# Optimization experiments

Hardware: AMD Instinct MI355X
Metric: run time of the kernel (lower is better)

Reference implementation:

```python
import jax, jax.numpy as jnp
import numpy as np

N_HEADS = 8
D_HEAD = 16
D_IN = 128
N_NODES = 50000
N_EDGES = 600000


def setup_inputs() -> dict:
    key = jax.random.key(0)
    ks = jax.random.split(key, 7)
    x = jax.random.normal(ks[0], (N_NODES, D_IN), dtype=jnp.float32)
    edge_attr = jax.random.normal(ks[1], (N_EDGES, D_IN), dtype=jnp.float32)
    edge_index = jax.random.randint(ks[2], (2, N_EDGES), 0, N_NODES, dtype=jnp.int32)
    # Linear weights stored as [in, out] so projection is x @ W.
    s = 1.0 / np.sqrt(D_IN)
    WQ = jax.random.normal(ks[3], (D_IN, N_HEADS * D_HEAD), dtype=jnp.float32) * s
    WK = jax.random.normal(ks[4], (D_IN, N_HEADS * D_HEAD), dtype=jnp.float32) * s
    WV = jax.random.normal(ks[5], (D_IN, N_HEADS * D_HEAD), dtype=jnp.float32) * s
    WE = jax.random.normal(ks[6], (D_IN, N_HEADS * D_HEAD), dtype=jnp.float32) * s
    return {"x": x, "edge_attr": edge_attr, "edge_index": edge_index,
            "WQ": WQ, "WK": WK, "WV": WV, "WE": WE}


def reference(x, edge_attr, edge_index, WQ, WK, WV, WE):
    N = x.shape[0]
    q = (x @ WQ).reshape(N, N_HEADS, D_HEAD)
    k = (x @ WK).reshape(N, N_HEADS, D_HEAD)
    v = (x @ WV).reshape(N, N_HEADS, D_HEAD)
    e_proj = (edge_attr @ WE).reshape(-1, N_HEADS, D_HEAD)
    row, col = edge_index[0], edge_index[1]
    # per-edge gather-compute: [E, H, D]
    alpha = (k[row] * q[col]) * (1.0 / np.sqrt(D_HEAD))
    alpha = jnp.clip(alpha, -5.0, 5.0) * e_proj
    e_out = alpha  # update_edge_feats=True
    alphax = jnp.exp(jnp.clip(alpha.sum(-1, keepdims=True), -5.0, 5.0))  # [E, H, 1]
    wV = jax.ops.segment_sum(v[row] * alphax, col, num_segments=N)  # [N, H, D]
    z = jax.ops.segment_sum(alphax, col, num_segments=N)            # [N, H, 1]
    h_out = wV / (z + 1e-6)
    return h_out, e_out
```

## Files before the change

### kernel.cpp

```cpp
#include <hip/hip_runtime.h>

#define DIN 128
#define NHEADS 8
#define DHEAD 16
#define NPB 32
#define EPB 64

typedef __attribute__((ext_vector_type(8))) short short8;
typedef __attribute__((ext_vector_type(4))) float f32x4;

__device__ __forceinline__ float clip5(float x) {
    return fminf(fmaxf(x, -5.0f), 5.0f);
}

__device__ __forceinline__ unsigned short f2bf(float f) {
    unsigned u = __float_as_uint(f);
    unsigned r = (u + 0x7FFF + ((u >> 16) & 1)) >> 16;
    return (unsigned short)r;
}

__device__ __forceinline__ float b2f(unsigned short u) {
    return __uint_as_float((unsigned)u << 16);
}

__device__ __forceinline__ float bflo(unsigned u) {
    return __uint_as_float(u << 16);
}
__device__ __forceinline__ float bfhi(unsigned u) {
    return __uint_as_float(u & 0xffff0000u);
}


__device__ __forceinline__ void tile_gemm(const float xs[][DIN], int r0, int cg,
                                          const float* __restrict__ W,
                                          float4 acc[4]) {
#pragma unroll 4
    for (int kk = 0; kk < DIN; kk += 4) {
        float4 a[4];
#pragma unroll
        for (int i = 0; i < 4; ++i)
            a[i] = *(const float4*)&xs[r0 + i][kk];
#pragma unroll
        for (int t = 0; t < 4; ++t) {
            float4 w = *(const float4*)&W[(kk + t) * DIN + (cg << 2)];
#pragma unroll
            for (int i = 0; i < 4; ++i) {
                float av = ((const float*)&a[i])[t];
                acc[i].x = fmaf(av, w.x, acc[i].x);
                acc[i].y = fmaf(av, w.y, acc[i].y);
                acc[i].z = fmaf(av, w.z, acc[i].z);
                acc[i].w = fmaf(av, w.w, acc[i].w);
            }
        }
    }
}

__global__ __launch_bounds__(256) void node_proj_kernel(
    const float* __restrict__ x, const float* __restrict__ WQ,
    const float* __restrict__ WK, const float* __restrict__ WV,
    unsigned short* __restrict__ qbf, unsigned short* __restrict__ kbf,
    unsigned short* __restrict__ vbf, int N) {
    __shared__ float xs[NPB][DIN];
    const int tid = threadIdx.x;
    const int n0 = blockIdx.x * NPB;

#pragma unroll
    for (int i = 0; i < NPB * DIN / (256 * 4); ++i) {
        int idx = (tid + i * 256) * 4;
        int r = idx / DIN, c = idx % DIN;
        float4 val = make_float4(0.f, 0.f, 0.f, 0.f);
        if (n0 + r < N) val = *(const float4*)&x[(long)(n0 + r) * DIN + c];
        *(float4*)&xs[r][c] = val;
    }
    __syncthreads();

    const int cg = tid & 31;
    const int ng = tid >> 5;
    const int r0 = ng * 4;

    const float* Ws[3] = {WQ, WK, WV};
    unsigned short* outs[3] = {qbf, kbf, vbf};
#pragma unroll
    for (int m = 0; m < 3; ++m) {
        float4 acc[4] = {make_float4(0,0,0,0), make_float4(0,0,0,0),
                         make_float4(0,0,0,0), make_float4(0,0,0,0)};
        tile_gemm(xs, r0, cg, Ws[m], acc);
#pragma unroll
        for (int i = 0; i < 4; ++i) {
            int n = n0 + r0 + i;
            if (n < N) {
                ushort4 b;
                b.x = f2bf(acc[i].x); b.y = f2bf(acc[i].y);
                b.z = f2bf(acc[i].z); b.w = f2bf(acc[i].w);
                *(ushort4*)&outs[m][(long)n * DIN + (cg << 2)] = b;
            }
        }
    }
}


__global__ __launch_bounds__(256) void degree_kernel(
    const int* __restrict__ cols, int* __restrict__ deg, int E) {
    int e = blockIdx.x * 256 + threadIdx.x;
    if (e < E) atomicAdd(&deg[cols[e]], 1);
}

__global__ __launch_bounds__(256) void block_sum_kernel(
    const int* __restrict__ deg, int* __restrict__ bsum, int N) {
    __shared__ int s[256];
    int tid = threadIdx.x;
    int i = blockIdx.x * 256 + tid;
    s[tid] = (i < N) ? deg[i] : 0;
    __syncthreads();
    for (int st = 128; st > 0; st >>= 1) {
        if (tid < st) s[tid] += s[tid + st];
        __syncthreads();
    }
    if (tid == 0) bsum[blockIdx.x] = s[0];
}

__global__ __launch_bounds__(256) void scan_bsum_kernel(int* __restrict__ bsum, int NB) {
    __shared__ int s[256];
    int tid = threadIdx.x;
    int v = (tid < NB) ? bsum[tid] : 0;
    s[tid] = v;
    __syncthreads();
    for (int off = 1; off < 256; off <<= 1) {
        int t = (tid >= off) ? s[tid - off] : 0;
        __syncthreads();
        s[tid] += t;
        __syncthreads();
    }
    if (tid < NB) bsum[tid] = s[tid] - v;
}

__global__ __launch_bounds__(256) void offsets_kernel(
    const int* __restrict__ deg, const int* __restrict__ bsumscan,
    int* __restrict__ offsets, int* __restrict__ cursor, int N, int E) {
    __shared__ int s[256];
    int tid = threadIdx.x;
    int i = blockIdx.x * 256 + tid;
    int v = (i < N) ? deg[i] : 0;
    s[tid] = v;
    __syncthreads();
    for (int off = 1; off < 256; off <<= 1) {
        int t = (tid >= off) ? s[tid - off] : 0;
        __syncthreads();
        s[tid] += t;
        __syncthreads();
    }
    int excl = s[tid] - v + bsumscan[blockIdx.x];
    if (i < N) { offsets[i] = excl; cursor[i] = excl; }
    if (blockIdx.x == 0 && tid == 0) offsets[N] = E;
}

__global__ __launch_bounds__(256) void scatter_kernel(
    const int* __restrict__ rows, const int* __restrict__ cols,
    int* __restrict__ cursor, int* __restrict__ elist,
    int* __restrict__ rows_s, int* __restrict__ cols_s, int E) {
    int e = blockIdx.x * 256 + threadIdx.x;
    if (e >= E) return;
    int c = cols[e];
    int pos = atomicAdd(&cursor[c], 1);
    elist[pos] = e;
    rows_s[pos] = rows[e];
    cols_s[pos] = c;
}


__global__ __launch_bounds__(256) void prep_wet_kernel(
    const float* __restrict__ WE, unsigned short* __restrict__ WEt) {
    int idx = blockIdx.x * 256 + threadIdx.x;
    int kk = idx >> 7, n = idx & 127;
    WEt[n * DIN + kk] = f2bf(WE[kk * DIN + n]);
}


__global__ __launch_bounds__(256) void edge_mfma_kernel(
    const float* __restrict__ edge_attr, const int* __restrict__ elist,
    const int* __restrict__ rows_s, const int* __restrict__ cols_s,
    const unsigned short* __restrict__ WEt, const unsigned short* __restrict__ qbf,
    const unsigned short* __restrict__ kbf, float* __restrict__ e_out,
    float* __restrict__ ax_s, int E) {
    const int tid = threadIdx.x;
    const int e0 = blockIdx.x * EPB;
    const int w = tid >> 6;
    const int l = tid & 63;
    const int lr = l & 15;
    const int lg = l >> 4;
    const int j = e0 + w * 16 + lr;
    const long eg = elist[j];
    const int er = rows_s[j];
    const int ec = cols_s[j];

    const float* arow = &edge_attr[eg * DIN + lg * 8];
    f32x4 ea[8];
#pragma unroll
    for (int ks = 0; ks < 4; ++ks) {
        ea[ks * 2]     = __builtin_nontemporal_load((const f32x4*)&arow[ks * 32]);
        ea[ks * 2 + 1] = __builtin_nontemporal_load((const f32x4*)&arow[ks * 32 + 4]);
    }
    const unsigned short* krow = &kbf[(long)er * DIN + lg * 4];
    const unsigned short* qrow = &qbf[(long)ec * DIN + lg * 4];
    ushort4 kv[8], qv[8];
#pragma unroll
    for (int ft = 0; ft < 8; ++ft) {
        kv[ft] = *(const ushort4*)&krow[ft * 16];
        qv[ft] = *(const ushort4*)&qrow[ft * 16];
    }
    __builtin_amdgcn_sched_barrier(0);

    short8 bfrag[4];
#pragma unroll
    for (int ks = 0; ks < 4; ++ks) {
        f32x4 a0 = ea[ks * 2], a1 = ea[ks * 2 + 1];
        short8 f;
        f[0] = (short)f2bf(a0[0]); f[1] = (short)f2bf(a0[1]);
        f[2] = (short)f2bf(a0[2]); f[3] = (short)f2bf(a0[3]);
        f[4] = (short)f2bf(a1[0]); f[5] = (short)f2bf(a1[1]);
        f[6] = (short)f2bf(a1[2]); f[7] = (short)f2bf(a1[3]);
        bfrag[ks] = f;
    }

#pragma unroll
    for (int ft = 0; ft < 8; ++ft) {
        f32x4 acc = (f32x4){0.f, 0.f, 0.f, 0.f};
#pragma unroll
        for (int ks = 0; ks < 4; ++ks) {
            short8 af = *(const short8*)&WEt[(ft * 16 + lr) * DIN + ks * 32 + lg * 8];
            acc = __builtin_amdgcn_mfma_f32_16x16x32_bf16(af, bfrag[ks], acc, 0, 0, 0);
        }
        const int f0 = ft * 16 + lg * 4;
        f32x4 t;
        t[0] = clip5(b2f(kv[ft].x) * b2f(qv[ft].x) * 0.25f) * acc[0];
        t[1] = clip5(b2f(kv[ft].y) * b2f(qv[ft].y) * 0.25f) * acc[1];
        t[2] = clip5(b2f(kv[ft].z) * b2f(qv[ft].z) * 0.25f) * acc[2];
        t[3] = clip5(b2f(kv[ft].w) * b2f(qv[ft].w) * 0.25f) * acc[3];
        __builtin_nontemporal_store(t, (f32x4*)&e_out[eg * DIN + f0]);

        float s = t[0] + t[1] + t[2] + t[3];
        s += __shfl_xor(s, 16);
        s += __shfl_xor(s, 32);
        float axv = __expf(clip5(s));
        if (lg == 0)
            ax_s[(long)j * NHEADS + ft] = axv;
    }
}


__global__ __launch_bounds__(256) void aggregate_kernel(
    const int* __restrict__ offsets, const int* __restrict__ rows_s,
    const float* __restrict__ ax_s, const unsigned short* __restrict__ vbf,
    float* __restrict__ h_out, int N) {
    int wid = blockIdx.x * 4 + (threadIdx.x >> 6);
    int lane = threadIdx.x & 63;
    if (wid >= N) return;
    int beg = offsets[wid], end = offsets[wid + 1];
    const int head = lane >> 3;

    float2 acc = make_float2(0.f, 0.f);
    float zacc = 0.f;

    for (int j = beg; j < end; j += 8) {
        int n = end - j; n = (n > 8) ? 8 : n;
        int r_[8]; float a_[8]; unsigned u_[8];
#pragma unroll
        for (int t = 0; t < 8; ++t)
            r_[t] = rows_s[j + ((t < n) ? t : 0)];
#pragma unroll
        for (int t = 0; t < 8; ++t) {
            a_[t] = (t < n) ? ax_s[(long)(j + t) * NHEADS + head] : 0.f;
            u_[t] = *(const unsigned*)&vbf[(long)r_[t] * DIN + lane * 2];
        }
#pragma unroll
        for (int t = 0; t < 8; ++t) {
            acc.x = fmaf(bflo(u_[t]), a_[t], acc.x);
            acc.y = fmaf(bfhi(u_[t]), a_[t], acc.y);
            zacc += a_[t];
        }
    }
    float inv = 1.0f / (zacc + 1e-6f);
    float2 res = make_float2(acc.x * inv, acc.y * inv);
    *(float2*)&h_out[(long)wid * DIN + lane * 2] = res;
}

extern "C" void kernel_launch(void* const* d_in, const int* in_sizes, int n_in,
                              void* d_out, int out_size, void* d_ws, size_t ws_size,
                              hipStream_t stream) {
    const float* x         = (const float*)d_in[0];
    const float* edge_attr = (const float*)d_in[1];
    const int*   edge_index= (const int*)d_in[2];
    const float* WQ        = (const float*)d_in[3];
    const float* WK        = (const float*)d_in[4];
    const float* WV        = (const float*)d_in[5];
    const float* WE        = (const float*)d_in[6];

    const int N = in_sizes[0] / DIN;
    const int E = in_sizes[2] / 2;
    const int NB = (N + 255) / 256;

    float* out   = (float*)d_out;
    float* h_out = out;
    float* e_out = out + (long)N * DIN;

    unsigned short* qbf = (unsigned short*)d_ws;
    unsigned short* kbf = qbf + (long)N * DIN;
    unsigned short* vbf = kbf + (long)N * DIN;
    float* ax_s = (float*)(vbf + (long)N * DIN);
    unsigned short* WEt = (unsigned short*)(ax_s + (long)E * NHEADS);
    int* ip      = (int*)(WEt + DIN * DIN);
    int* deg     = ip;
    int* cursor  = deg + N;
    int* offsets = cursor + N;
    int* bsum    = offsets + N + 1;
    int* elist   = bsum + 256;
    int* rows_s  = elist + E;
    int* cols_s  = rows_s + E;

    const int* rows = edge_index;
    const int* cols = edge_index + E;

    hipMemsetAsync(deg, 0, (size_t)N * sizeof(int), stream);

    node_proj_kernel<<<(N + NPB - 1) / NPB, 256, 0, stream>>>(x, WQ, WK, WV, qbf, kbf, vbf, N);
    prep_wet_kernel<<<DIN * DIN / 256, 256, 0, stream>>>(WE, WEt);

    degree_kernel<<<(E + 255) / 256, 256, 0, stream>>>(cols, deg, E);
    block_sum_kernel<<<NB, 256, 0, stream>>>(deg, bsum, N);
    scan_bsum_kernel<<<1, 256, 0, stream>>>(bsum, NB);
    offsets_kernel<<<NB, 256, 0, stream>>>(deg, bsum, offsets, cursor, N, E);
    scatter_kernel<<<(E + 255) / 256, 256, 0, stream>>>(rows, cols, cursor,
                                                        elist, rows_s, cols_s, E);

    edge_mfma_kernel<<<E / EPB, 256, 0, stream>>>(
        edge_attr, elist, rows_s, cols_s, WEt, qbf, kbf, e_out, ax_s, E);

    aggregate_kernel<<<(N + 3) / 4, 256, 0, stream>>>(
        offsets, rows_s, ax_s, vbf, h_out, N);
}
```

Measured before the change: 485.7 us.

## Software-pipeline edge MFMA kernel over four 16-edge chunks per wave

Each wave now handles 64 edges in four chunks of 16, double-buffering registers so the gathers of edge_attr, K and Q for the next chunk are issued while the current chunk runs its MFMA and epilogue. Index loads are prefetched two chunks ahead, and the block size per launch grows from 64 to 256 edges, with launch bounds asking for two blocks per SIMD. The aim is to hide gather latency inside each wave instead of relying on occupancy. The cost is higher register pressure from the double buffers, which could cause spills or lower occupancy, plus fewer blocks in the grid.

```diff
diff --git a/kernel.cpp b/kernel.cpp
--- a/kernel.cpp
+++ b/kernel.cpp
@@ -4,7 +4,7 @@
 #define NHEADS 8
 #define DHEAD 16
 #define NPB 32
-#define EPB 64
+#define EPB 256
 
 typedef __attribute__((ext_vector_type(8))) short short8;
 typedef __attribute__((ext_vector_type(4))) float f32x4;
@@ -176,7 +176,7 @@
 }
 
 
-__global__ __launch_bounds__(256) void edge_mfma_kernel(
+__global__ __launch_bounds__(256, 2) void edge_mfma_kernel(
     const float* __restrict__ edge_attr, const int* __restrict__ elist,
     const int* __restrict__ rows_s, const int* __restrict__ cols_s,
     const unsigned short* __restrict__ WEt, const unsigned short* __restrict__ qbf,
@@ -188,63 +188,96 @@
     const int l = tid & 63;
     const int lr = l & 15;
     const int lg = l >> 4;
-    const int j = e0 + w * 16 + lr;
-    const long eg = elist[j];
-    const int er = rows_s[j];
-    const int ec = cols_s[j];
-
-    const float* arow = &edge_attr[eg * DIN + lg * 8];
-    f32x4 ea[8];
-#pragma unroll
-    for (int ks = 0; ks < 4; ++ks) {
-        ea[ks * 2]     = __builtin_nontemporal_load((const f32x4*)&arow[ks * 32]);
-        ea[ks * 2 + 1] = __builtin_nontemporal_load((const f32x4*)&arow[ks * 32 + 4]);
-    }
-    const unsigned short* krow = &kbf[(long)er * DIN + lg * 4];
-    const unsigned short* qrow = &qbf[(long)ec * DIN + lg * 4];
-    ushort4 kv[8], qv[8];
-#pragma unroll
-    for (int ft = 0; ft < 8; ++ft) {
-        kv[ft] = *(const ushort4*)&krow[ft * 16];
-        qv[ft] = *(const ushort4*)&qrow[ft * 16];
-    }
+    const int jbase = e0 + w * 64;
+
+    bool valid[4];
+    int eg_[4], er_[4], ec_[4];
+    f32x4 ea_[2][8];
+    ushort4 kv_[2][8], qv_[2][8];
+
+#pragma unroll
+    for (int c = 0; c < 4; ++c) valid[c] = (jbase + c * 16) < E;
+
+#define IDX_LOAD(c)                                                  \
+    if (valid[c]) {                                                  \
+        int j = jbase + (c) * 16 + lr;                               \
+        eg_[c] = elist[j]; er_[c] = rows_s[j]; ec_[c] = cols_s[j];   \
+    }
+
+#define DATA_LOAD(s, c)                                              \
+    if (valid[c]) {                                                  \
+        const float* arow = &edge_attr[(long)eg_[c] * DIN + lg * 8]; \
+        _Pragma("unroll")                                            \
+        for (int ks = 0; ks < 4; ++ks) {                             \
+            ea_[s][ks * 2]     = __builtin_nontemporal_load((const f32x4*)&arow[ks * 32]);     \
+            ea_[s][ks * 2 + 1] = __builtin_nontemporal_load((const f32x4*)&arow[ks * 32 + 4]); \
+        }                                                            \
+        const unsigned short* krow = &kbf[(long)er_[c] * DIN + lg * 4]; \
+        const unsigned short* qrow = &qbf[(long)ec_[c] * DIN + lg * 4]; \
+        _Pragma("unroll")                                            \
+        for (int ft = 0; ft < 8; ++ft) {                             \
+            kv_[s][ft] = *(const ushort4*)&krow[ft * 16];            \
+            qv_[s][ft] = *(const ushort4*)&qrow[ft * 16];            \
+        }                                                            \
+    }
+
+    IDX_LOAD(0)
+    IDX_LOAD(1)
     __builtin_amdgcn_sched_barrier(0);
-
-    short8 bfrag[4];
-#pragma unroll
-    for (int ks = 0; ks < 4; ++ks) {
-        f32x4 a0 = ea[ks * 2], a1 = ea[ks * 2 + 1];
-        short8 f;
-        f[0] = (short)f2bf(a0[0]); f[1] = (short)f2bf(a0[1]);
-        f[2] = (short)f2bf(a0[2]); f[3] = (short)f2bf(a0[3]);
-        f[4] = (short)f2bf(a1[0]); f[5] = (short)f2bf(a1[1]);
-        f[6] = (short)f2bf(a1[2]); f[7] = (short)f2bf(a1[3]);
-        bfrag[ks] = f;
-    }
-
-#pragma unroll
-    for (int ft = 0; ft < 8; ++ft) {
-        f32x4 acc = (f32x4){0.f, 0.f, 0.f, 0.f};
-#pragma unroll
-        for (int ks = 0; ks < 4; ++ks) {
-            short8 af = *(const short8*)&WEt[(ft * 16 + lr) * DIN + ks * 32 + lg * 8];
-            acc = __builtin_amdgcn_mfma_f32_16x16x32_bf16(af, bfrag[ks], acc, 0, 0, 0);
-        }
-        const int f0 = ft * 16 + lg * 4;
-        f32x4 t;
-        t[0] = clip5(b2f(kv[ft].x) * b2f(qv[ft].x) * 0.25f) * acc[0];
-        t[1] = clip5(b2f(kv[ft].y) * b2f(qv[ft].y) * 0.25f) * acc[1];
-        t[2] = clip5(b2f(kv[ft].z) * b2f(qv[ft].z) * 0.25f) * acc[2];
-        t[3] = clip5(b2f(kv[ft].w) * b2f(qv[ft].w) * 0.25f) * acc[3];
-        __builtin_nontemporal_store(t, (f32x4*)&e_out[eg * DIN + f0]);
-
-        float s = t[0] + t[1] + t[2] + t[3];
-        s += __shfl_xor(s, 16);
-        s += __shfl_xor(s, 32);
-        float axv = __expf(clip5(s));
-        if (lg == 0)
-            ax_s[(long)j * NHEADS + ft] = axv;
-    }
+    DATA_LOAD(0, 0)
+    __builtin_amdgcn_sched_barrier(0);
+
+#pragma unroll
+    for (int c = 0; c < 4; ++c) {
+        const int s = c & 1;
+        if (c + 2 < 4) { IDX_LOAD(c + 2) }
+        if (c + 1 < 4) { DATA_LOAD((c + 1) & 1, c + 1) }
+        __builtin_amdgcn_sched_barrier(0);
+
+        if (valid[c]) {
+            const int j = jbase + c * 16 + lr;
+            const long eg = eg_[c];
+
+            short8 bfrag[4];
+#pragma unroll
+            for (int ks = 0; ks < 4; ++ks) {
+                f32x4 a0 = ea_[s][ks * 2], a1 = ea_[s][ks * 2 + 1];
+                short8 f;
+                f[0] = (short)f2bf(a0[0]); f[1] = (short)f2bf(a0[1]);
+                f[2] = (short)f2bf(a0[2]); f[3] = (short)f2bf(a0[3]);
+                f[4] = (short)f2bf(a1[0]); f[5] = (short)f2bf(a1[1]);
+                f[6] = (short)f2bf(a1[2]); f[7] = (short)f2bf(a1[3]);
+                bfrag[ks] = f;
+            }
+
+#pragma unroll
+            for (int ft = 0; ft < 8; ++ft) {
+                f32x4 acc = (f32x4){0.f, 0.f, 0.f, 0.f};
+#pragma unroll
+                for (int ks = 0; ks < 4; ++ks) {
+                    short8 af = *(const short8*)&WEt[(ft * 16 + lr) * DIN + ks * 32 + lg * 8];
+                    acc = __builtin_amdgcn_mfma_f32_16x16x32_bf16(af, bfrag[ks], acc, 0, 0, 0);
+                }
+                const int f0 = ft * 16 + lg * 4;
+                f32x4 t;
+                t[0] = clip5(b2f(kv_[s][ft].x) * b2f(qv_[s][ft].x) * 0.25f) * acc[0];
+                t[1] = clip5(b2f(kv_[s][ft].y) * b2f(qv_[s][ft].y) * 0.25f) * acc[1];
+                t[2] = clip5(b2f(kv_[s][ft].z) * b2f(qv_[s][ft].z) * 0.25f) * acc[2];
+                t[3] = clip5(b2f(kv_[s][ft].w) * b2f(qv_[s][ft].w) * 0.25f) * acc[3];
+                __builtin_nontemporal_store(t, (f32x4*)&e_out[eg * DIN + f0]);
+
+                float sum = t[0] + t[1] + t[2] + t[3];
+                sum += __shfl_xor(sum, 16);
+                sum += __shfl_xor(sum, 32);
+                float axv = __expf(clip5(sum));
+                if (lg == 0)
+                    ax_s[(long)j * NHEADS + ft] = axv;
+            }
+        }
+        __builtin_amdgcn_sched_barrier(0);
+    }
+#undef IDX_LOAD
+#undef DATA_LOAD
 }
 
 
@@ -332,7 +365,7 @@
     scatter_kernel<<<(E + 255) / 256, 256, 0, stream>>>(rows, cols, cursor,
                                                         elist, rows_s, cols_s, E);
 
-    edge_mfma_kernel<<<E / EPB, 256, 0, stream>>>(
+    edge_mfma_kernel<<<(E + EPB - 1) / EPB, 256, 0, stream>>>(
         edge_attr, elist, rows_s, cols_s, WEt, qbf, kbf, e_out, ax_s, E);
 
     aggregate_kernel<<<(N + 3) / 4, 256, 0, stream>>>(
```

Result: slower. 500.6 us (+3.1%).

## Split aggregate wave into four edge sub-groups with 16-byte V loads

Applied to the files above, without the earlier changes.

The aggregation kernel now has each wave split into four 16-lane sub-groups. Each sub-group handles different edges of the node and loads a full 16-byte chunk of the bf16 V row per lane, instead of all 64 lanes reading 4 bytes from the same edge. Partial sums are combined with cross-lane shuffles, and one sub-group writes the output, which adds an early path for nodes with no edges. The aim is fewer, wider gather loads and fewer serial loop iterations per node, at the cost of a shuffle reduction and idle lanes during the store.

```diff
diff --git a/kernel.cpp b/kernel.cpp
--- a/kernel.cpp
+++ b/kernel.cpp
@@ -256,32 +256,60 @@
     int lane = threadIdx.x & 63;
     if (wid >= N) return;
     int beg = offsets[wid], end = offsets[wid + 1];
-    const int head = lane >> 3;
-
-    float2 acc = make_float2(0.f, 0.f);
+    const int sub = lane >> 4;
+    const int f16 = lane & 15;
+    const int head = f16 >> 1;
+
+    if (beg == end) {
+        if (sub == 0) {
+            f32x4 zz = (f32x4){0.f, 0.f, 0.f, 0.f};
+            *(f32x4*)&h_out[(long)wid * DIN + f16 * 8] = zz;
+            *(f32x4*)&h_out[(long)wid * DIN + f16 * 8 + 4] = zz;
+        }
+        return;
+    }
+
+    float acc[8] = {0.f, 0.f, 0.f, 0.f, 0.f, 0.f, 0.f, 0.f};
     float zacc = 0.f;
 
     for (int j = beg; j < end; j += 8) {
-        int n = end - j; n = (n > 8) ? 8 : n;
-        int r_[8]; float a_[8]; unsigned u_[8];
-#pragma unroll
-        for (int t = 0; t < 8; ++t)
-            r_[t] = rows_s[j + ((t < n) ? t : 0)];
-#pragma unroll
-        for (int t = 0; t < 8; ++t) {
-            a_[t] = (t < n) ? ax_s[(long)(j + t) * NHEADS + head] : 0.f;
-            u_[t] = *(const unsigned*)&vbf[(long)r_[t] * DIN + lane * 2];
-        }
-#pragma unroll
-        for (int t = 0; t < 8; ++t) {
-            acc.x = fmaf(bflo(u_[t]), a_[t], acc.x);
-            acc.y = fmaf(bfhi(u_[t]), a_[t], acc.y);
-            zacc += a_[t];
-        }
-    }
-    float inv = 1.0f / (zacc + 1e-6f);
-    float2 res = make_float2(acc.x * inv, acc.y * inv);
-    *(float2*)&h_out[(long)wid * DIN + lane * 2] = res;
+        int n = end - j;
+        bool v0 = sub < n, v1 = 4 + sub < n;
+        int jj0 = v0 ? (j + sub) : beg;
+        int jj1 = v1 ? (j + 4 + sub) : beg;
+        int r0 = rows_s[jj0], r1 = rows_s[jj1];
+        float a0 = v0 ? ax_s[(long)jj0 * NHEADS + head] : 0.f;
+        float a1 = v1 ? ax_s[(long)jj1 * NHEADS + head] : 0.f;
+        uint4 u0 = *(const uint4*)&vbf[(long)r0 * DIN + f16 * 8];
+        uint4 u1 = *(const uint4*)&vbf[(long)r1 * DIN + f16 * 8];
+
+        acc[0] = fmaf(bflo(u0.x), a0, acc[0]); acc[1] = fmaf(bfhi(u0.x), a0, acc[1]);
+        acc[2] = fmaf(bflo(u0.y), a0, acc[2]); acc[3] = fmaf(bfhi(u0.y), a0, acc[3]);
+        acc[4] = fmaf(bflo(u0.z), a0, acc[4]); acc[5] = fmaf(bfhi(u0.z), a0, acc[5]);
+        acc[6] = fmaf(bflo(u0.w), a0, acc[6]); acc[7] = fmaf(bfhi(u0.w), a0, acc[7]);
+        zacc += a0;
+        acc[0] = fmaf(bflo(u1.x), a1, acc[0]); acc[1] = fmaf(bfhi(u1.x), a1, acc[1]);
+        acc[2] = fmaf(bflo(u1.y), a1, acc[2]); acc[3] = fmaf(bfhi(u1.y), a1, acc[3]);
+        acc[4] = fmaf(bflo(u1.z), a1, acc[4]); acc[5] = fmaf(bfhi(u1.z), a1, acc[5]);
+        acc[6] = fmaf(bflo(u1.w), a1, acc[6]); acc[7] = fmaf(bfhi(u1.w), a1, acc[7]);
+        zacc += a1;
+    }
+
+#pragma unroll
+    for (int i = 0; i < 8; ++i) {
+        acc[i] += __shfl_xor(acc[i], 16);
+        acc[i] += __shfl_xor(acc[i], 32);
+    }
+    zacc += __shfl_xor(zacc, 16);
+    zacc += __shfl_xor(zacc, 32);
+
+    if (sub == 0) {
+        float inv = 1.0f / (zacc + 1e-6f);
+        f32x4 r0 = (f32x4){acc[0] * inv, acc[1] * inv, acc[2] * inv, acc[3] * inv};
+        f32x4 r1 = (f32x4){acc[4] * inv, acc[5] * inv, acc[6] * inv, acc[7] * inv};
+        *(f32x4*)&h_out[(long)wid * DIN + f16 * 8] = r0;
+        *(f32x4*)&h_out[(long)wid * DIN + f16 * 8 + 4] = r1;
+    }
 }
 
 extern "C" void kernel_launch(void* const* d_in, const int* in_sizes, int n_in,
```

New measurement: 484.1 us. About the same (-0.3%).
